# Kernel optimization log

Measured on AMD Instinct MI355X. Metric: run time of the kernel, lower is better.

Reference implementation:

```python
import jax, jax.numpy as jnp
import numpy as np

D_MODEL = 1024
N_HEADS = 16
HEAD_D = D_MODEL // N_HEADS  # 64
B, T = 4, 4096
ROPE_BASE = 10000.0


def _rope(x):
    # Standard interleaved RoPE over the full feature dim (module applies RoPE
    # to q,k after reshaping back to (B,T,D)).
    Bx, Tx, Dx = x.shape
    half = Dx // 2
    inv_freq = 1.0 / (ROPE_BASE ** (jnp.arange(half, dtype=jnp.float32) / half))
    ang = jnp.arange(Tx, dtype=jnp.float32)[:, None] * inv_freq[None, :]  # (T, half)
    cos, sin = jnp.cos(ang), jnp.sin(ang)
    x1 = x[..., 0::2]
    x2 = x[..., 1::2]
    r1 = x1 * cos - x2 * sin
    r2 = x1 * sin + x2 * cos
    # interleave back
    out = jnp.stack([r1, r2], axis=-1).reshape(Bx, Tx, Dx)
    return out


def setup_inputs() -> dict:
    key = jax.random.key(0)
    k_x, k_q, k_k, k_v = jax.random.split(key, 4)
    x = jax.random.normal(k_x, (B, T, D_MODEL), dtype=jnp.float32)
    # kaiming_uniform on (d, d, n_heads): fan_in = d*n_heads, bound = sqrt(6/fan_in)
    bound = np.sqrt(6.0 / (HEAD_D * N_HEADS))
    shp = (HEAD_D, HEAD_D, N_HEADS)
    w_q = jax.random.uniform(k_q, shp, jnp.float32, -bound, bound)
    w_k = jax.random.uniform(k_k, shp, jnp.float32, -bound, bound)
    w_v = jax.random.uniform(k_v, shp, jnp.float32, -bound, bound)
    return {"x": x, "w_q": w_q, "w_k": w_k, "w_v": w_v}


def reference(x, w_q, w_k, w_v):
    Bx, Tx, Dx = x.shape
    d = Dx // N_HEADS
    xh = x.reshape(Bx, Tx, d, N_HEADS)  # (B,T,d,h)
    q = jnp.einsum('btqh,qdh->btdh', xh, w_q).reshape(Bx, Tx, Dx)
    k = jnp.einsum('btkh,kdh->btdh', xh, w_k).reshape(Bx, Tx, Dx)
    v = jnp.einsum('btvh,vdh->btdh', xh, w_v).reshape(Bx, Tx, Dx)
    q = _rope(q)
    k = _rope(k)
    gamma = 1.0 / jnp.sqrt(jnp.float32(Dx))
    scores = jnp.einsum('bqd,bkd->bqk', q, k) * gamma  # contracts FULL D (single map)
    causal = jnp.tril(jnp.ones((Tx, Tx), dtype=bool))
    scores = jnp.where(causal[None], scores, -jnp.inf)
    attn = jax.nn.softmax(scores, axis=-1)
    y = jnp.einsum('bqt,btd->bqd', attn, v)
    return y
```

## Files before the change

kernel.cpp:

```cpp
#include <hip/hip_runtime.h>
#include <cmath>

#define B_ 4
#define T_ 4096
#define D_ 1024

typedef __attribute__((ext_vector_type(4))) float f32x4;
typedef __attribute__((ext_vector_type(2))) float f32x2;
typedef __attribute__((ext_vector_type(8))) short s16x8;

__device__ __forceinline__ f32x4 mfma_bf16(s16x8 a, s16x8 b, f32x4 c) {
    return __builtin_amdgcn_mfma_f32_16x16x32_bf16(a, b, c, 0, 0, 0);
}
__device__ __forceinline__ unsigned short f2bf(float f) {
    union { float f; unsigned int u; } v; v.f = f;
    unsigned int r = v.u + 0x7FFFu + ((v.u >> 16) & 1u);
    return (unsigned short)(r >> 16);
}
template <int CTRL>
__device__ __forceinline__ float dppf(float x) {
    return __int_as_float(
        __builtin_amdgcn_mov_dpp(__float_as_int(x), CTRL, 0xF, 0xF, true));
}
__device__ __forceinline__ float rowmax16(float v) {
    v = fmaxf(v, dppf<0xB1>(v));
    v = fmaxf(v, dppf<0x4E>(v));
    v = fmaxf(v, dppf<0x141>(v));
    v = fmaxf(v, dppf<0x140>(v));
    return v;
}
__device__ __forceinline__ float rowsum16(float v) {
    v += dppf<0xB1>(v);
    v += dppf<0x4E>(v);
    v += dppf<0x141>(v);
    v += dppf<0x140>(v);
    return v;
}

__global__ __launch_bounds__(256) void k_wtrans(const float* __restrict__ wq,
                                                const float* __restrict__ wk,
                                                const float* __restrict__ wv,
                                                unsigned short* __restrict__ wt) {
    int p = blockIdx.x >> 4;
    int h = blockIdx.x & 15;
    const float* src = (p == 0) ? wq : (p == 1) ? wk : wv;
    unsigned short* dst = wt + (size_t)((p * 16 + h) * 64) * 64;
    for (int idx = threadIdx.x; idx < 64 * 64; idx += 256) {
        int d = idx >> 6, i = idx & 63;
        dst[d * 64 + i] = f2bf(src[i * 1024 + d * 16 + h]);
    }
}

__global__ __launch_bounds__(256, 3) void k_qkv(const float* __restrict__ x,
                                             const unsigned short* __restrict__ wt,
                                             unsigned short* __restrict__ Qt,
                                             unsigned short* __restrict__ Kt,
                                             unsigned short* __restrict__ Vt) {
    int bid = blockIdx.x;
    int hp  = bid >> 8;
    int b   = (bid >> 6) & 3;
    int tc  = bid & 63;
    int t0  = tc * 64;
    int tid = threadIdx.x, w = tid >> 6, lane = tid & 63;
    int quad = lane >> 4, l16 = lane & 15;

    __shared__ alignas(16) unsigned short xh[2 * 64 * 72];
    __shared__ alignas(16) unsigned short outl[64 * 68];

    for (int n = tid; n < 4096; n += 256) {
        int t = n >> 6, i = n & 63;
        f32x2 v = *(const f32x2*)&x[(size_t)(b * T_ + t0 + t) * D_ + i * 16 + 2 * hp];
        xh[t * 72 + i]        = f2bf(v.x);
        xh[4608 + t * 72 + i] = f2bf(v.y);
    }
    __syncthreads();

    s16x8 xf[2][2];
    #pragma unroll
    for (int hh = 0; hh < 2; ++hh)
        #pragma unroll
        for (int kc = 0; kc < 2; ++kc)
            xf[hh][kc] = *(const s16x8*)&xh[hh * 4608 + (16 * w + l16) * 72 + kc * 32 + quad * 8];

    f32x4 acc[3][2][4];
    #pragma unroll
    for (int p = 0; p < 3; ++p)
        #pragma unroll
        for (int hh = 0; hh < 2; ++hh)
            #pragma unroll
            for (int nt = 0; nt < 4; ++nt)
                acc[p][hh][nt] = (f32x4){0.f, 0.f, 0.f, 0.f};

    #pragma unroll
    for (int p = 0; p < 3; ++p)
        #pragma unroll
        for (int hh = 0; hh < 2; ++hh)
            #pragma unroll
            for (int nt = 0; nt < 4; ++nt)
                #pragma unroll
                for (int kc = 0; kc < 2; ++kc) {
                    const s16x8 wf = *(const s16x8*)&wt[
                        (size_t)((p * 16 + 2 * hp + hh) * 64 + nt * 16 + l16) * 64 + kc * 32 + quad * 8];
                    if (p < 2)
                        acc[p][hh][nt] = mfma_bf16(xf[hh][kc], wf, acc[p][hh][nt]);
                    else
                        acc[p][hh][nt] = mfma_bf16(wf, xf[hh][kc], acc[p][hh][nt]);
                }

    #pragma unroll
    for (int nt = 0; nt < 4; ++nt) {
        int d = nt * 16 + l16;
        float f = exp2f((float)(d * 8 + hp) * -0.02595256324130751f);
        #pragma unroll
        for (int r = 0; r < 4; ++r) {
            float ang = (float)(t0 + 16 * w + quad * 4 + r) * f;
            float s, c;
            sincosf(ang, &s, &c);
            float a0 = acc[0][0][nt][r], a1 = acc[0][1][nt][r];
            acc[0][0][nt][r] = a0 * c - a1 * s;
            acc[0][1][nt][r] = a0 * s + a1 * c;
            float k0 = acc[1][0][nt][r], k1 = acc[1][1][nt][r];
            acc[1][0][nt][r] = k0 * c - k1 * s;
            acc[1][1][nt][r] = k0 * s + k1 * c;
        }
    }

    #pragma unroll
    for (int p = 0; p < 3; ++p)
        #pragma unroll
        for (int hh = 0; hh < 2; ++hh) {
            __syncthreads();
            if (p < 2) {
                #pragma unroll
                for (int nt = 0; nt < 4; ++nt)
                    #pragma unroll
                    for (int r = 0; r < 4; ++r)
                        outl[(16 * w + quad * 4 + r) * 68 + nt * 16 + l16] = f2bf(acc[p][hh][nt][r]);
            } else {
                #pragma unroll
                for (int mt = 0; mt < 4; ++mt)
                    #pragma unroll
                    for (int r = 0; r < 4; ++r)
                        outl[(mt * 16 + quad * 4 + r) * 68 + 16 * w + l16] = f2bf(acc[p][hh][mt][r]);
            }
            __syncthreads();
            int h = 2 * hp + hh;
            if (p < 2) {
                unsigned short* g = (p == 0 ? Qt : Kt) + ((size_t)(b * 16 + h) * T_ + t0) * 64;
                for (int n = 2 * tid; n < 4096; n += 512) {
                    int t = n >> 6, dd = n & 63;
                    *(unsigned int*)(g + n) = *(const unsigned int*)&outl[t * 68 + dd];
                }
            } else {
                unsigned short* g = Vt + (size_t)(b * 16 + h) * 64 * T_;
                for (int n = 2 * tid; n < 4096; n += 512) {
                    int d = n >> 6, tt = n & 63;
                    int tile = 2 * tc + (tt >> 5);
                    *(unsigned int*)(g + (size_t)tile * 2048 + d * 32 + (tt & 31)) =
                        *(const unsigned int*)&outl[d * 68 + tt];
                }
            }
        }
}

__global__ __launch_bounds__(512, 2) void k_attn(const unsigned short* __restrict__ Qt,
                                              const unsigned short* __restrict__ Kt,
                                              const unsigned short* __restrict__ Vt,
                                              float* __restrict__ out) {
    int bid = blockIdx.x;
    int b = (bid >> 1) & 3;
    int q = ((bid >> 3) & 31) * 2 + (bid & 1);
    int qt = (bid < 256) ? (127 - q) : q;
    int q0 = qt * 32;
    int tid = threadIdx.x, w = tid >> 6, lane = tid & 63;
    int quad = lane >> 4, l16 = lane & 15;

    __shared__ alignas(16) float S_red[8][32][68];
    __shared__ alignas(16) unsigned short P_lds[32][72];
    __shared__ float alpha_s[32], l_st[32];

    s16x8 qf[2][4];
    #pragma unroll
    for (int qs = 0; qs < 2; ++qs)
        #pragma unroll
        for (int c = 0; c < 4; ++c) {
            int dg = w * 128 + c * 32 + quad * 8;
            int head = dg >> 6, d64 = dg & 63;
            qf[qs][c] = *(const s16x8*)&Qt[((size_t)(b * 16 + head) * T_ + q0 + qs * 16 + l16) * 64 + d64];
        }

    f32x4 Y[8][2];
    #pragma unroll
    for (int mt = 0; mt < 8; ++mt) { Y[mt][0] = (f32x4){0,0,0,0}; Y[mt][1] = (f32x4){0,0,0,0}; }

    const float gamma = 0.03125f;
    int rq = tid >> 4;
    int kk4 = (tid & 15) * 4;
    int nkt = (qt >> 1) + 1;
    float m_reg = -INFINITY, l_reg = 0.f;

    {
        f32x4 S[4][2];
        #pragma unroll
        for (int kps = 0; kps < 4; ++kps) { S[kps][0] = (f32x4){0,0,0,0}; S[kps][1] = (f32x4){0,0,0,0}; }
        #pragma unroll
        for (int kps = 0; kps < 4; ++kps)
            #pragma unroll
            for (int c = 0; c < 4; ++c) {
                int dg = w * 128 + c * 32 + quad * 8;
                int head = dg >> 6, d64 = dg & 63;
                s16x8 kf = *(const s16x8*)&Kt[((size_t)(b * 16 + head) * T_ + kps * 16 + l16) * 64 + d64];
                S[kps][0] = mfma_bf16(kf, qf[0][c], S[kps][0]);
                S[kps][1] = mfma_bf16(kf, qf[1][c], S[kps][1]);
            }
        #pragma unroll
        for (int kps = 0; kps < 4; ++kps)
            #pragma unroll
            for (int qs = 0; qs < 2; ++qs)
                *(f32x4*)&S_red[w][qs * 16 + l16][kps * 16 + quad * 4] = S[kps][qs];
    }
    __syncthreads();

    s16x8 vfA[8];
    s16x8 vfB[8];

    for (int kt = 0; kt < nkt; ++kt) {
        int kbase = kt * 64;
        bool more = (kt + 1 < nkt);

        #pragma unroll
        for (int mt = 0; mt < 8; ++mt) {
            int dg = w * 128 + mt * 16 + l16;
            int head = dg >> 6, d64 = dg & 63;
            vfA[mt] = *(const s16x8*)&Vt[
                (((size_t)(b * 16 + head) * 128 + 2 * kt) * 64 + d64) * 32 + quad * 8];
        }

        f32x4 s = {0.f, 0.f, 0.f, 0.f};
        #pragma unroll
        for (int sl = 0; sl < 8; ++sl) {
            f32x4 v = *(const f32x4*)&S_red[sl][rq][kk4];
            s.x += v.x; s.y += v.y; s.z += v.z; s.w += v.w;
        }
        int qg = q0 + rq;
        int kb = kbase + kk4;
        s.x = (kb     > qg) ? -INFINITY : s.x * gamma;
        s.y = (kb + 1 > qg) ? -INFINITY : s.y * gamma;
        s.z = (kb + 2 > qg) ? -INFINITY : s.z * gamma;
        s.w = (kb + 3 > qg) ? -INFINITY : s.w * gamma;
        float mx = rowmax16(fmaxf(fmaxf(s.x, s.y), fmaxf(s.z, s.w)));
        float m_new = fmaxf(m_reg, mx);
        float alpha = __expf(m_reg - m_new);
        float p0 = __expf(s.x - m_new), p1 = __expf(s.y - m_new);
        float p2 = __expf(s.z - m_new), p3 = __expf(s.w - m_new);
        float ps = rowsum16((p0 + p1) + (p2 + p3));
        l_reg = alpha * l_reg + ps;
        m_reg = m_new;
        if ((tid & 15) == 0) alpha_s[rq] = alpha;
        unsigned int plo = (unsigned int)f2bf(p0) | ((unsigned int)f2bf(p1) << 16);
        unsigned int phi = (unsigned int)f2bf(p2) | ((unsigned int)f2bf(p3) << 16);
        *(unsigned long long*)&P_lds[rq][kk4] =
            (unsigned long long)plo | ((unsigned long long)phi << 32);
        __syncthreads();

        #pragma unroll
        for (int mt = 0; mt < 8; ++mt) {
            int dg = w * 128 + mt * 16 + l16;
            int head = dg >> 6, d64 = dg & 63;
            vfB[mt] = *(const s16x8*)&Vt[
                (((size_t)(b * 16 + head) * 128 + 2 * kt + 1) * 64 + d64) * 32 + quad * 8];
        }
        float a0 = alpha_s[l16], a1 = alpha_s[16 + l16];
        s16x8 pf0a = *(const s16x8*)&P_lds[l16][quad * 8];
        s16x8 pf0b = *(const s16x8*)&P_lds[l16][32 + quad * 8];
        s16x8 pf1a = *(const s16x8*)&P_lds[16 + l16][quad * 8];
        s16x8 pf1b = *(const s16x8*)&P_lds[16 + l16][32 + quad * 8];
        int scale = __any((a0 < 1.f) || (a1 < 1.f));
        __builtin_amdgcn_s_setprio(1);
        if (scale) {
            #pragma unroll
            for (int mt = 0; mt < 8; ++mt) { Y[mt][0] *= a0; Y[mt][1] *= a1; }
        }
        #pragma unroll
        for (int mt = 0; mt < 8; ++mt) {
            Y[mt][0] = mfma_bf16(vfA[mt], pf0a, Y[mt][0]);
            Y[mt][1] = mfma_bf16(vfA[mt], pf1a, Y[mt][1]);
        }
        #pragma unroll
        for (int mt = 0; mt < 8; ++mt) {
            Y[mt][0] = mfma_bf16(vfB[mt], pf0b, Y[mt][0]);
            Y[mt][1] = mfma_bf16(vfB[mt], pf1b, Y[mt][1]);
        }
        if (more) {
            f32x4 S[4][2];
            #pragma unroll
            for (int kps = 0; kps < 4; ++kps) { S[kps][0] = (f32x4){0,0,0,0}; S[kps][1] = (f32x4){0,0,0,0}; }
            #pragma unroll
            for (int kps = 0; kps < 4; ++kps)
                #pragma unroll
                for (int c = 0; c < 4; ++c) {
                    int dg = w * 128 + c * 32 + quad * 8;
                    int head = dg >> 6, d64 = dg & 63;
                    s16x8 kf = *(const s16x8*)&Kt[
                        ((size_t)(b * 16 + head) * T_ + kbase + 64 + kps * 16 + l16) * 64 + d64];
                    S[kps][0] = mfma_bf16(kf, qf[0][c], S[kps][0]);
                    S[kps][1] = mfma_bf16(kf, qf[1][c], S[kps][1]);
                }
            #pragma unroll
            for (int kps = 0; kps < 4; ++kps)
                #pragma unroll
                for (int qs = 0; qs < 2; ++qs)
                    *(f32x4*)&S_red[w][qs * 16 + l16][kps * 16 + quad * 4] = S[kps][qs];
        }
        __builtin_amdgcn_s_setprio(0);
        __syncthreads();
    }

    if ((tid & 15) == 0) l_st[rq] = l_reg;
    __syncthreads();
    float inv0 = 1.f / l_st[l16], inv1 = 1.f / l_st[16 + l16];
    #pragma unroll
    for (int mt = 0; mt < 8; ++mt)
        #pragma unroll
        for (int r = 0; r < 4; ++r) {
            int dg = w * 128 + mt * 16 + quad * 4 + r;
            int head = dg >> 6, d64 = dg & 63;
            int e = d64 * 16 + head;
            out[(size_t)(b * T_ + q0 + l16) * D_ + e]      = Y[mt][0][r] * inv0;
            out[(size_t)(b * T_ + q0 + 16 + l16) * D_ + e] = Y[mt][1][r] * inv1;
        }
}

extern "C" void kernel_launch(void* const* d_in, const int* in_sizes, int n_in,
                              void* d_out, int out_size, void* d_ws, size_t ws_size,
                              hipStream_t stream) {
    const float* x  = (const float*)d_in[0];
    const float* wq = (const float*)d_in[1];
    const float* wk = (const float*)d_in[2];
    const float* wv = (const float*)d_in[3];
    unsigned short* ws = (unsigned short*)d_ws;

    const size_t WT_ELEMS  = 3 * 16 * 64 * 64;
    const size_t QKV_ELEMS = (size_t)B_ * 16 * T_ * 64;
    const size_t NEED_BYTES = (WT_ELEMS + 3 * QKV_ELEMS) * sizeof(unsigned short);
    if (ws_size < NEED_BYTES) return;

    unsigned short* wt = ws;
    unsigned short* Qt = ws + WT_ELEMS;
    unsigned short* Kt = Qt + QKV_ELEMS;
    unsigned short* Vt = Kt + QKV_ELEMS;
    float* outp = (float*)d_out;

    k_wtrans<<<48, 256, 0, stream>>>(wq, wk, wv, wt);
    k_qkv<<<2048, 256, 0, stream>>>(x, wt, Qt, Kt, Vt);
    k_attn<<<512, 512, 0, stream>>>(Qt, Kt, Vt, outp);
}
```

Measured before the change: 709.6 us.

## Split KV range across two wavegroups per block with flash-decoding style merge

The attention kernel now launches 256 blocks of 1024 threads. Each block processes two query tiles, paired from opposite ends of the causal triangle to balance load, in two sequential passes. Within a block, two 512-thread groups take alternating 32-key tiles, and each keeps its own online softmax state. The groups' partial outputs are then merged through shared memory by rescaling with the combined max. This aims to add parallelism along the key dimension and balance work, at the cost of extra barriers, a shared-memory merge, smaller per-step tiles and a launch bound of 1024 threads.

After: 2.460 ms. 3.47x slower.

```diff
diff --git a/kernel.cpp b/kernel.cpp
--- a/kernel.cpp
+++ b/kernel.cpp
@@ -163,172 +163,197 @@
         }
 }
 
-__global__ __launch_bounds__(512, 2) void k_attn(const unsigned short* __restrict__ Qt,
-                                              const unsigned short* __restrict__ Kt,
-                                              const unsigned short* __restrict__ Vt,
-                                              float* __restrict__ out) {
+__global__ __launch_bounds__(1024, 4) void k_attn(const unsigned short* __restrict__ Qt,
+                                                  const unsigned short* __restrict__ Kt,
+                                                  const unsigned short* __restrict__ Vt,
+                                                  float* __restrict__ out) {
     int bid = blockIdx.x;
     int b = (bid >> 1) & 3;
-    int q = ((bid >> 3) & 31) * 2 + (bid & 1);
-    int qt = (bid < 256) ? (127 - q) : q;
-    int q0 = qt * 32;
-    int tid = threadIdx.x, w = tid >> 6, lane = tid & 63;
-    int quad = lane >> 4, l16 = lane & 15;
-
-    __shared__ alignas(16) float S_red[8][32][68];
-    __shared__ alignas(16) unsigned short P_lds[32][72];
-    __shared__ float alpha_s[32], l_st[32];
-
-    s16x8 qf[2][4];
-    #pragma unroll
-    for (int qs = 0; qs < 2; ++qs)
-        #pragma unroll
-        for (int c = 0; c < 4; ++c) {
-            int dg = w * 128 + c * 32 + quad * 8;
-            int head = dg >> 6, d64 = dg & 63;
-            qf[qs][c] = *(const s16x8*)&Qt[((size_t)(b * 16 + head) * T_ + q0 + qs * 16 + l16) * 64 + d64];
-        }
-
-    f32x4 Y[8][2];
-    #pragma unroll
-    for (int mt = 0; mt < 8; ++mt) { Y[mt][0] = (f32x4){0,0,0,0}; Y[mt][1] = (f32x4){0,0,0,0}; }
+    int j = ((bid >> 3) << 1) | (bid & 1);
+    int tid = threadIdx.x;
+    int g = tid >> 9;
+    int gtid = tid & 511;
+    int w = gtid >> 6;
+    int quad = (tid >> 4) & 3, l16 = tid & 15;
+    int rq = gtid >> 4;
+    int kk = l16 * 2;
+
+    __shared__ alignas(16) float S_red[2][8][32][36];
+    __shared__ alignas(16) unsigned short P_lds[2][32][40];
+    __shared__ float alpha_s[2][32];
+    __shared__ float m_pub[2][32], l_pub[2][32];
 
     const float gamma = 0.03125f;
-    int rq = tid >> 4;
-    int kk4 = (tid & 15) * 4;
-    int nkt = (qt >> 1) + 1;
-    float m_reg = -INFINITY, l_reg = 0.f;
-
-    {
-        f32x4 S[4][2];
-        #pragma unroll
-        for (int kps = 0; kps < 4; ++kps) { S[kps][0] = (f32x4){0,0,0,0}; S[kps][1] = (f32x4){0,0,0,0}; }
-        #pragma unroll
-        for (int kps = 0; kps < 4; ++kps)
+
+    #pragma unroll 1
+    for (int pass = 0; pass < 2; ++pass) {
+        int qt = pass ? j : 127 - j;
+        int q0 = qt * 32;
+        int nkt = qt + 1;
+        int nsA = (nkt + 1) >> 1, nsB = nkt >> 1;
+        int ns = g ? nsB : nsA;
+        int nIv = (2 * nsA > 2 * nsB + 1) ? 2 * nsA : 2 * nsB + 1;
+
+        s16x8 qf[2][4];
+        #pragma unroll
+        for (int qs = 0; qs < 2; ++qs)
             #pragma unroll
             for (int c = 0; c < 4; ++c) {
                 int dg = w * 128 + c * 32 + quad * 8;
                 int head = dg >> 6, d64 = dg & 63;
-                s16x8 kf = *(const s16x8*)&Kt[((size_t)(b * 16 + head) * T_ + kps * 16 + l16) * 64 + d64];
-                S[kps][0] = mfma_bf16(kf, qf[0][c], S[kps][0]);
-                S[kps][1] = mfma_bf16(kf, qf[1][c], S[kps][1]);
-            }
-        #pragma unroll
-        for (int kps = 0; kps < 4; ++kps)
+                qf[qs][c] = *(const s16x8*)&Qt[((size_t)(b * 16 + head) * T_ + q0 + qs * 16 + l16) * 64 + d64];
+            }
+
+        f32x4 Y[8][2];
+        #pragma unroll
+        for (int mt = 0; mt < 8; ++mt) { Y[mt][0] = (f32x4){0,0,0,0}; Y[mt][1] = (f32x4){0,0,0,0}; }
+        float m_reg = -INFINITY, l_reg = 0.f;
+
+        if (ns > 0) {
             #pragma unroll
-            for (int qs = 0; qs < 2; ++qs)
-                *(f32x4*)&S_red[w][qs * 16 + l16][kps * 16 + quad * 4] = S[kps][qs];
-    }
-    __syncthreads();
-
-    s16x8 vfA[8];
-    s16x8 vfB[8];
-
-    for (int kt = 0; kt < nkt; ++kt) {
-        int kbase = kt * 64;
-        bool more = (kt + 1 < nkt);
-
-        #pragma unroll
-        for (int mt = 0; mt < 8; ++mt) {
-            int dg = w * 128 + mt * 16 + l16;
-            int head = dg >> 6, d64 = dg & 63;
-            vfA[mt] = *(const s16x8*)&Vt[
-                (((size_t)(b * 16 + head) * 128 + 2 * kt) * 64 + d64) * 32 + quad * 8];
-        }
-
-        f32x4 s = {0.f, 0.f, 0.f, 0.f};
-        #pragma unroll
-        for (int sl = 0; sl < 8; ++sl) {
-            f32x4 v = *(const f32x4*)&S_red[sl][rq][kk4];
-            s.x += v.x; s.y += v.y; s.z += v.z; s.w += v.w;
-        }
-        int qg = q0 + rq;
-        int kb = kbase + kk4;
-        s.x = (kb     > qg) ? -INFINITY : s.x * gamma;
-        s.y = (kb + 1 > qg) ? -INFINITY : s.y * gamma;
-        s.z = (kb + 2 > qg) ? -INFINITY : s.z * gamma;
-        s.w = (kb + 3 > qg) ? -INFINITY : s.w * gamma;
-        float mx = rowmax16(fmaxf(fmaxf(s.x, s.y), fmaxf(s.z, s.w)));
-        float m_new = fmaxf(m_reg, mx);
-        float alpha = __expf(m_reg - m_new);
-        float p0 = __expf(s.x - m_new), p1 = __expf(s.y - m_new);
-        float p2 = __expf(s.z - m_new), p3 = __expf(s.w - m_new);
-        float ps = rowsum16((p0 + p1) + (p2 + p3));
-        l_reg = alpha * l_reg + ps;
-        m_reg = m_new;
-        if ((tid & 15) == 0) alpha_s[rq] = alpha;
-        unsigned int plo = (unsigned int)f2bf(p0) | ((unsigned int)f2bf(p1) << 16);
-        unsigned int phi = (unsigned int)f2bf(p2) | ((unsigned int)f2bf(p3) << 16);
-        *(unsigned long long*)&P_lds[rq][kk4] =
-            (unsigned long long)plo | ((unsigned long long)phi << 32);
-        __syncthreads();
-
-        #pragma unroll
-        for (int mt = 0; mt < 8; ++mt) {
-            int dg = w * 128 + mt * 16 + l16;
-            int head = dg >> 6, d64 = dg & 63;
-            vfB[mt] = *(const s16x8*)&Vt[
-                (((size_t)(b * 16 + head) * 128 + 2 * kt + 1) * 64 + d64) * 32 + quad * 8];
-        }
-        float a0 = alpha_s[l16], a1 = alpha_s[16 + l16];
-        s16x8 pf0a = *(const s16x8*)&P_lds[l16][quad * 8];
-        s16x8 pf0b = *(const s16x8*)&P_lds[l16][32 + quad * 8];
-        s16x8 pf1a = *(const s16x8*)&P_lds[16 + l16][quad * 8];
-        s16x8 pf1b = *(const s16x8*)&P_lds[16 + l16][32 + quad * 8];
-        int scale = __any((a0 < 1.f) || (a1 < 1.f));
-        __builtin_amdgcn_s_setprio(1);
-        if (scale) {
-            #pragma unroll
-            for (int mt = 0; mt < 8; ++mt) { Y[mt][0] *= a0; Y[mt][1] *= a1; }
-        }
-        #pragma unroll
-        for (int mt = 0; mt < 8; ++mt) {
-            Y[mt][0] = mfma_bf16(vfA[mt], pf0a, Y[mt][0]);
-            Y[mt][1] = mfma_bf16(vfA[mt], pf1a, Y[mt][1]);
-        }
-        #pragma unroll
-        for (int mt = 0; mt < 8; ++mt) {
-            Y[mt][0] = mfma_bf16(vfB[mt], pf0b, Y[mt][0]);
-            Y[mt][1] = mfma_bf16(vfB[mt], pf1b, Y[mt][1]);
-        }
-        if (more) {
-            f32x4 S[4][2];
-            #pragma unroll
-            for (int kps = 0; kps < 4; ++kps) { S[kps][0] = (f32x4){0,0,0,0}; S[kps][1] = (f32x4){0,0,0,0}; }
-            #pragma unroll
-            for (int kps = 0; kps < 4; ++kps)
+            for (int kps = 0; kps < 2; ++kps) {
+                f32x4 S0 = (f32x4){0,0,0,0}, S1 = (f32x4){0,0,0,0};
                 #pragma unroll
                 for (int c = 0; c < 4; ++c) {
                     int dg = w * 128 + c * 32 + quad * 8;
                     int head = dg >> 6, d64 = dg & 63;
-                    s16x8 kf = *(const s16x8*)&Kt[
-                        ((size_t)(b * 16 + head) * T_ + kbase + 64 + kps * 16 + l16) * 64 + d64];
-                    S[kps][0] = mfma_bf16(kf, qf[0][c], S[kps][0]);
-                    S[kps][1] = mfma_bf16(kf, qf[1][c], S[kps][1]);
-                }
-            #pragma unroll
-            for (int kps = 0; kps < 4; ++kps)
-                #pragma unroll
-                for (int qs = 0; qs < 2; ++qs)
-                    *(f32x4*)&S_red[w][qs * 16 + l16][kps * 16 + quad * 4] = S[kps][qs];
-        }
-        __builtin_amdgcn_s_setprio(0);
+                    s16x8 kf = *(const s16x8*)&Kt[((size_t)(b * 16 + head) * T_ + g * 32 + kps * 16 + l16) * 64 + d64];
+                    S0 = mfma_bf16(kf, qf[0][c], S0);
+                    S1 = mfma_bf16(kf, qf[1][c], S1);
+                }
+                *(f32x4*)&S_red[g][w][l16][kps * 16 + quad * 4] = S0;
+                *(f32x4*)&S_red[g][w][16 + l16][kps * 16 + quad * 4] = S1;
+            }
+        }
         __syncthreads();
+
+        s16x8 vfA[4];
+        s16x8 vfB[4];
+
+        for (int iv = 0; iv < nIv; ++iv) {
+            int ph = iv - g;
+            int s = ph >> 1;
+            bool act = (ph >= 0) && (s < ns);
+            if (act && !(ph & 1)) {
+                int tk = 2 * s + g;
+                #pragma unroll
+                for (int mt = 0; mt < 4; ++mt) {
+                    int dg = w * 128 + mt * 16 + l16;
+                    int head = dg >> 6, d64 = dg & 63;
+                    vfA[mt] = *(const s16x8*)&Vt[
+                        (((size_t)(b * 16 + head) * 128 + tk) * 64 + d64) * 32 + quad * 8];
+                }
+                float s0 = 0.f, s1 = 0.f;
+                #pragma unroll
+                for (int sl = 0; sl < 8; ++sl) {
+                    f32x2 v = *(const f32x2*)&S_red[g][sl][rq][kk];
+                    s0 += v.x; s1 += v.y;
+                }
+                int qg = q0 + rq;
+                int kb = tk * 32 + kk;
+                s0 = (kb     > qg) ? -INFINITY : s0 * gamma;
+                s1 = (kb + 1 > qg) ? -INFINITY : s1 * gamma;
+                float mx = rowmax16(fmaxf(s0, s1));
+                float m_new = fmaxf(m_reg, mx);
+                float alpha = __expf(m_reg - m_new);
+                float p0 = __expf(s0 - m_new), p1 = __expf(s1 - m_new);
+                float ps = rowsum16(p0 + p1);
+                l_reg = alpha * l_reg + ps;
+                m_reg = m_new;
+                if ((tid & 15) == 0) alpha_s[g][rq] = alpha;
+                unsigned int pp = (unsigned int)f2bf(p0) | ((unsigned int)f2bf(p1) << 16);
+                *(unsigned int*)&P_lds[g][rq][kk] = pp;
+            } else if (act) {
+                int tk = 2 * s + g;
+                #pragma unroll
+                for (int mt = 0; mt < 4; ++mt) {
+                    int dg = w * 128 + (mt + 4) * 16 + l16;
+                    int head = dg >> 6, d64 = dg & 63;
+                    vfB[mt] = *(const s16x8*)&Vt[
+                        (((size_t)(b * 16 + head) * 128 + tk) * 64 + d64) * 32 + quad * 8];
+                }
+                float a0 = alpha_s[g][l16], a1 = alpha_s[g][16 + l16];
+                s16x8 pf0 = *(const s16x8*)&P_lds[g][l16][quad * 8];
+                s16x8 pf1 = *(const s16x8*)&P_lds[g][16 + l16][quad * 8];
+                int scale = __any((a0 < 1.f) || (a1 < 1.f));
+                __builtin_amdgcn_s_setprio(1);
+                if (scale) {
+                    #pragma unroll
+                    for (int mt = 0; mt < 8; ++mt) { Y[mt][0] *= a0; Y[mt][1] *= a1; }
+                }
+                #pragma unroll
+                for (int mt = 0; mt < 4; ++mt) {
+                    Y[mt][0] = mfma_bf16(vfA[mt], pf0, Y[mt][0]);
+                    Y[mt][1] = mfma_bf16(vfA[mt], pf1, Y[mt][1]);
+                }
+                if (s + 1 < ns) {
+                    int kb2 = (tk + 2) * 32;
+                    #pragma unroll
+                    for (int kps = 0; kps < 2; ++kps) {
+                        f32x4 S0 = (f32x4){0,0,0,0}, S1 = (f32x4){0,0,0,0};
+                        #pragma unroll
+                        for (int c = 0; c < 4; ++c) {
+                            int dg = w * 128 + c * 32 + quad * 8;
+                            int head = dg >> 6, d64 = dg & 63;
+                            s16x8 kf = *(const s16x8*)&Kt[
+                                ((size_t)(b * 16 + head) * T_ + kb2 + kps * 16 + l16) * 64 + d64];
+                            S0 = mfma_bf16(kf, qf[0][c], S0);
+                            S1 = mfma_bf16(kf, qf[1][c], S1);
+                        }
+                        *(f32x4*)&S_red[g][w][l16][kps * 16 + quad * 4] = S0;
+                        *(f32x4*)&S_red[g][w][16 + l16][kps * 16 + quad * 4] = S1;
+                    }
+                }
+                #pragma unroll
+                for (int mt = 0; mt < 4; ++mt) {
+                    Y[mt + 4][0] = mfma_bf16(vfB[mt], pf0, Y[mt + 4][0]);
+                    Y[mt + 4][1] = mfma_bf16(vfB[mt], pf1, Y[mt + 4][1]);
+                }
+                __builtin_amdgcn_s_setprio(0);
+            }
+            __syncthreads();
+        }
+
+        if ((tid & 15) == 0) { m_pub[g][rq] = m_reg; l_pub[g][rq] = l_reg; }
+        __syncthreads();
+        float* mrg = &S_red[0][0][0][0];
+        #pragma unroll 1
+        for (int ck = 0; ck < 2; ++ck) {
+            if (g == 1 && (w >> 2) == ck) {
+                #pragma unroll
+                for (int mt = 0; mt < 8; ++mt)
+                    #pragma unroll
+                    for (int qs = 0; qs < 2; ++qs)
+                        #pragma unroll
+                        for (int r = 0; r < 4; ++r)
+                            mrg[((w & 3) * 32 + qs * 16 + l16) * 132 + mt * 16 + quad * 4 + r] = Y[mt][qs][r];
+            }
+            __syncthreads();
+            if (g == 0 && (w >> 2) == ck) {
+                #pragma unroll
+                for (int qs = 0; qs < 2; ++qs) {
+                    int q = qs * 16 + l16;
+                    float mA = m_pub[0][q], mB = m_pub[1][q];
+                    float m = fmaxf(mA, mB);
+                    float sA = __expf(mA - m);
+                    float sB = (mB == -INFINITY) ? 0.f : __expf(mB - m);
+                    float linv = 1.f / (sA * l_pub[0][q] + sB * l_pub[1][q]);
+                    #pragma unroll
+                    for (int mt = 0; mt < 8; ++mt)
+                        #pragma unroll
+                        for (int r = 0; r < 4; ++r) {
+                            float yb = mrg[((w & 3) * 32 + q) * 132 + mt * 16 + quad * 4 + r];
+                            float y = (sA * Y[mt][qs][r] + sB * yb) * linv;
+                            int dg = w * 128 + mt * 16 + quad * 4 + r;
+                            int head = dg >> 6, d64 = dg & 63;
+                            int e = d64 * 16 + head;
+                            out[(size_t)(b * T_ + q0 + q) * D_ + e] = y;
+                        }
+                }
+            }
+            __syncthreads();
+        }
     }
-
-    if ((tid & 15) == 0) l_st[rq] = l_reg;
-    __syncthreads();
-    float inv0 = 1.f / l_st[l16], inv1 = 1.f / l_st[16 + l16];
-    #pragma unroll
-    for (int mt = 0; mt < 8; ++mt)
-        #pragma unroll
-        for (int r = 0; r < 4; ++r) {
-            int dg = w * 128 + mt * 16 + quad * 4 + r;
-            int head = dg >> 6, d64 = dg & 63;
-            int e = d64 * 16 + head;
-            out[(size_t)(b * T_ + q0 + l16) * D_ + e]      = Y[mt][0][r] * inv0;
-            out[(size_t)(b * T_ + q0 + 16 + l16) * D_ + e] = Y[mt][1][r] * inv1;
-        }
 }
 
 extern "C" void kernel_launch(void* const* d_in, const int* in_sizes, int n_in,
@@ -353,5 +378,5 @@
 
     k_wtrans<<<48, 256, 0, stream>>>(wq, wk, wv, wt);
     k_qkv<<<2048, 256, 0, stream>>>(x, wt, Qt, Kt, Vt);
-    k_attn<<<512, 512, 0, stream>>>(Qt, Kt, Vt, outp);
-}
+    k_attn<<<256, 1024, 0, stream>>>(Qt, Kt, Vt, outp);
+}
```
